# Optimization experiments

Hardware: AMD Instinct MI355X
Metric: run time of the kernel (lower is better)

Reference implementation:

```python
import jax, jax.numpy as jnp
import numpy as np

N, E, G = 50000, 1600000, 64
IN, HID, OUT = 128, 64, 64
NEG_SLOPE = 0.2


def _p(key, shape):
    return jax.random.normal(key, shape, dtype=jnp.float32) * 0.1


def setup_inputs() -> dict:
    key = jax.random.key(0)
    ks = jax.random.split(key, 24)
    inp = {
        "x": jax.random.normal(ks[0], (N, IN), dtype=jnp.float32),
        "edge_index": jax.random.randint(ks[1], (2, E), 0, N),
        "edge_attr": jax.random.uniform(ks[2], (E, 1), dtype=jnp.float32),
        "batch": jnp.sort(jax.random.randint(ks[3], (N,), 0, G)),
        # GATv2 layer 1 (in=128 -> 64, heads=1)
        "Wl1": _p(ks[4], (IN, HID)), "bl1": _p(ks[5], (HID,)),
        "Wr1": _p(ks[6], (IN, HID)), "br1": _p(ks[7], (HID,)),
        "We1": _p(ks[8], (1, HID)), "att1": _p(ks[9], (HID,)), "bias1": _p(ks[10], (HID,)),
        # GATv2 layer 2 (64 -> 64)
        "Wl2": _p(ks[11], (HID, OUT)), "bl2": _p(ks[12], (OUT,)),
        "Wr2": _p(ks[13], (HID, OUT)), "br2": _p(ks[14], (OUT,)),
        "We2": _p(ks[15], (1, OUT)), "att2": _p(ks[16], (OUT,)), "bias2": _p(ks[17], (OUT,)),
        # MLP head: fc1 (64->32), bn1 (32), fc3 (32->1)
        "W_fc1": _p(ks[18], (OUT, OUT // 2)), "b_fc1": _p(ks[19], (OUT // 2,)),
        "bn_gamma": jnp.ones((OUT // 2,), jnp.float32),
        "bn_beta": jnp.zeros((OUT // 2,), jnp.float32),
        "bn_mean": _p(ks[20], (OUT // 2,)),
        "bn_var": jax.random.uniform(ks[21], (OUT // 2,), jnp.float32, 0.5, 1.5),
        "W_fc3": _p(ks[22], (OUT // 2, 1)), "b_fc3": _p(ks[23], (1,)),
    }
    return inp


def _add_self_loops(src, dst, edge_attr, n):
    # PyG add_self_loops with fill_value='mean': loop attr = mean of incoming edge attrs per node
    s = jax.ops.segment_sum(edge_attr, dst, num_segments=n)  # (N,1)
    c = jax.ops.segment_sum(jnp.ones((edge_attr.shape[0], 1), edge_attr.dtype), dst, num_segments=n)
    loop_attr = s / jnp.maximum(c, 1.0)
    loops = jnp.arange(n)
    return (jnp.concatenate([src, loops]), jnp.concatenate([dst, loops]),
            jnp.concatenate([edge_attr, loop_attr], axis=0))


def _gatv2(h, src, dst, e_attr, Wl, bl, Wr, br, We, att, bias, n):
    xl = h @ Wl + bl                     # (N, C) source transform
    xr = h @ Wr + br                     # (N, C) target transform
    ef = e_attr @ We                     # (E', C)
    s = jax.nn.leaky_relu(xl[src] + xr[dst] + ef, NEG_SLOPE)  # (E', C)
    logits = s @ att                     # (E',)
    m = jax.ops.segment_max(logits, dst, num_segments=n)
    m = jnp.where(jnp.isfinite(m), m, 0.0)
    p = jnp.exp(logits - m[dst])
    denom = jax.ops.segment_sum(p, dst, num_segments=n)
    alpha = p / (denom[dst] + 1e-16)
    out = jax.ops.segment_sum(alpha[:, None] * xl[src], dst, num_segments=n)
    return out + bias


def reference(x, edge_index, edge_attr, batch,
              Wl1, bl1, Wr1, br1, We1, att1, bias1,
              Wl2, bl2, Wr2, br2, We2, att2, bias2,
              W_fc1, b_fc1, bn_gamma, bn_beta, bn_mean, bn_var, W_fc3, b_fc3):
    n = x.shape[0]
    src, dst, ea = _add_self_loops(edge_index[0], edge_index[1], edge_attr, n)
    h = jax.nn.elu(_gatv2(x, src, dst, ea, Wl1, bl1, Wr1, br1, We1, att1, bias1, n))
    h = jax.nn.elu(_gatv2(h, src, dst, ea, Wl2, bl2, Wr2, br2, We2, att2, bias2, n))
    # global_mean_pool
    sums = jax.ops.segment_sum(h, batch, num_segments=G)
    cnts = jax.ops.segment_sum(jnp.ones((n, 1), h.dtype), batch, num_segments=G)
    pooled = sums / jnp.maximum(cnts, 1.0)
    # head: bn1(relu(fc1(.))) with eval-mode BN, dropout off, then fc3
    z = jax.nn.relu(pooled @ W_fc1 + b_fc1)
    z = (z - bn_mean) / jnp.sqrt(bn_var + 1e-5) * bn_gamma + bn_beta
    return z @ W_fc3 + b_fc3
```

## Files before the change

kernel.cpp:

```cpp
#include <hip/hip_runtime.h>
#include <hip/hip_fp16.h>
#include <math.h>

typedef unsigned long long u64;
typedef __attribute__((ext_vector_type(2))) _Float16 half2v;
typedef __attribute__((ext_vector_type(4))) _Float16 half4v;
typedef __attribute__((ext_vector_type(8))) _Float16 half8;
typedef __attribute__((ext_vector_type(4))) float f32x4;
typedef __attribute__((ext_vector_type(2))) float f32x2;


#define BKT     256
#define CAP     12032
#define MAXSPAN 13056
#define PEPB    4096
#define NPWP    64

__global__ void k_prep_w(const float* __restrict__ Wl1, const float* __restrict__ bl1,
                         const float* __restrict__ Wr1, const float* __restrict__ br1,
                         const float* __restrict__ Wl2, const float* __restrict__ bl2,
                         const float* __restrict__ Wr2, const float* __restrict__ br2,
                         _Float16* __restrict__ Wt1, float* __restrict__ bv1,
                         _Float16* __restrict__ Wt2, float* __restrict__ bv2, int ld1) {
    int t = blockIdx.x * blockDim.x + threadIdx.x;
    int stride = gridDim.x * blockDim.x;
    int IN1 = 1 << ld1;
    for (int i = t; i < 128 * IN1; i += stride) {
        int n = i >> ld1, k = i & (IN1 - 1);
        float v = (n < 64) ? Wl1[k * 64 + n] : Wr1[k * 64 + (n - 64)];
        Wt1[n * IN1 + k] = (_Float16)v;
    }
    for (int i = t; i < 128 * 64; i += stride) {
        int n = i >> 6, k = i & 63;
        float v = (n < 64) ? Wl2[k * 64 + n] : Wr2[k * 64 + (n - 64)];
        Wt2[n * 64 + k] = (_Float16)v;
    }
    if (t < 128) {
        bv1[t] = (t < 64) ? bl1[t] : br1[t - 64];
        bv2[t] = (t < 64) ? bl2[t] : br2[t - 64];
    }
}

template<int IN>
__device__ __forceinline__ void xf_block_mfma(
        const float* __restrict__ h,
        const _Float16* __restrict__ Wt,
        const float* __restrict__ bv,
        __half* __restrict__ xl, __half* __restrict__ xr,
        int N, int node0, _Float16* rows, int t) {
    constexpr int LDK = IN + 8;
    constexpr int Q = IN / 4;
    for (int idx = t; idx < 64 * Q; idx += 256) {
        int nn = idx / Q;
        int kk = (idx % Q) * 4;
        int node = node0 + nn;
        float4 v = {0.f, 0.f, 0.f, 0.f};
        if (node < N) v = *(const float4*)(h + (size_t)node * IN + kk);
        half4v hv = {(_Float16)v.x, (_Float16)v.y, (_Float16)v.z, (_Float16)v.w};
        *(half4v*)(rows + nn * LDK + kk) = hv;
    }
    __syncthreads();
    int lane = t & 63, w = t >> 6;
    int n0w = w * 32;
    int lr = lane & 15, lq = lane >> 4;
    f32x4 acc[4][2];
#pragma unroll
    for (int i = 0; i < 4; ++i)
#pragma unroll
        for (int j = 0; j < 2; ++j) acc[i][j] = {0.f, 0.f, 0.f, 0.f};
    const _Float16* arow = rows + lr * LDK + lq * 8;
    const _Float16* brow = Wt + (size_t)(n0w + lr) * IN + lq * 8;
#pragma unroll
    for (int k0 = 0; k0 < IN; k0 += 32) {
        half8 a0 = *(const half8*)(arow + k0);
        half8 a1 = *(const half8*)(arow + 16 * LDK + k0);
        half8 a2 = *(const half8*)(arow + 32 * LDK + k0);
        half8 a3 = *(const half8*)(arow + 48 * LDK + k0);
        half8 b0 = *(const half8*)(brow + k0);
        half8 b1 = *(const half8*)(brow + 16 * IN + k0);
        acc[0][0] = __builtin_amdgcn_mfma_f32_16x16x32_f16(a0, b0, acc[0][0], 0, 0, 0);
        acc[1][0] = __builtin_amdgcn_mfma_f32_16x16x32_f16(a1, b0, acc[1][0], 0, 0, 0);
        acc[2][0] = __builtin_amdgcn_mfma_f32_16x16x32_f16(a2, b0, acc[2][0], 0, 0, 0);
        acc[3][0] = __builtin_amdgcn_mfma_f32_16x16x32_f16(a3, b0, acc[3][0], 0, 0, 0);
        acc[0][1] = __builtin_amdgcn_mfma_f32_16x16x32_f16(a0, b1, acc[0][1], 0, 0, 0);
        acc[1][1] = __builtin_amdgcn_mfma_f32_16x16x32_f16(a1, b1, acc[1][1], 0, 0, 0);
        acc[2][1] = __builtin_amdgcn_mfma_f32_16x16x32_f16(a2, b1, acc[2][1], 0, 0, 0);
        acc[3][1] = __builtin_amdgcn_mfma_f32_16x16x32_f16(a3, b1, acc[3][1], 0, 0, 0);
    }
    float bia0 = bv[n0w + lr];
    float bia1 = bv[n0w + 16 + lr];
#pragma unroll
    for (int ni = 0; ni < 2; ++ni) {
        int dim = n0w + ni * 16 + lr;
        __half* dst = (dim < 64) ? xl : xr;
        int dd = dim & 63;
        float bb = ni ? bia1 : bia0;
#pragma unroll
        for (int mi = 0; mi < 4; ++mi) {
#pragma unroll
            for (int r = 0; r < 4; ++r) {
                int node = node0 + mi * 16 + lq * 4 + r;
                if (node < N)
                    dst[((size_t)node << 6) + dd] = __float2half(acc[mi][ni][r] + bb);
            }
        }
    }
}

union XfPartSmem {
    _Float16 rows[64 * 136];
    struct { int lh[256]; int lbase[256]; int lcur[256]; } p;
};

template<int IN>
__global__ void k_xf1_part(
        const float* __restrict__ h,
        const _Float16* __restrict__ Wt, const float* __restrict__ bv,
        __half* __restrict__ xl, __half* __restrict__ xr, int N, int nbXF,
        const int* __restrict__ ei, const float* __restrict__ ea,
        int* __restrict__ qtail, u64* __restrict__ queue, int E) {
    __shared__ XfPartSmem sm;
    int t = threadIdx.x;
    if (blockIdx.x < nbXF) {
        xf_block_mfma<IN>(h, Wt, bv, xl, xr, N, blockIdx.x * 64, sm.rows, t);
    } else {
        int pb = blockIdx.x - nbXF;
        sm.p.lh[t] = 0; sm.p.lcur[t] = 0;
        __syncthreads();
        int base = pb * PEPB;
        int end = base + PEPB; if (end > E) end = E;
        for (int e = base + t; e < end; e += 256) {
            int d = ei[E + e];
            atomicAdd(&sm.p.lh[d >> 8], 1);
        }
        __syncthreads();
        if (sm.p.lh[t]) sm.p.lbase[t] = atomicAdd(&qtail[t], sm.p.lh[t]);
        __syncthreads();
        for (int e = base + t; e < end; e += 256) {
            int d = ei[E + e];
            int src = ei[e];
            float a = ea[e];
            int b = d >> 8;
            int idx = atomicAdd(&sm.p.lcur[b], 1);
            unsigned aq = (unsigned)(a * 16777216.0f);
            queue[(size_t)b * CAP + sm.p.lbase[b] + idx] =
                (((u64)aq) << 25) | (((u64)(d & 255)) << 17) | (unsigned)src;
        }
    }
}

__device__ __forceinline__ unsigned attr_q15(float a) {
    unsigned short hb = __builtin_bit_cast(unsigned short, (_Float16)a);
    return (unsigned)(hb >> 1);
}

__global__ void __launch_bounds__(1024)
k_build(const u64* __restrict__ queue, const int* __restrict__ qtail,
        u64* __restrict__ rs2, unsigned* __restrict__ csr, int N) {
    __shared__ u64 stat[BKT];
    __shared__ int fill[BKT], sc[BKT];
    __shared__ unsigned lcsr[MAXSPAN];
    int t = threadIdx.x, b = blockIdx.x;
    if (t < BKT) stat[t] = 0;
    __syncthreads();
    int cnt = qtail[b];
    size_t q0 = (size_t)b * CAP;
    for (int i = t; i < cnt; i += 1024) {
        u64 r = queue[q0 + i];
        int dl = (int)((r >> 17) & (BKT - 1));
        atomicAdd(&stat[dl], (1ULL << 32) | (unsigned)(r >> 25));
    }
    __syncthreads();
    int dg = b * BKT + t;
    u64 p = (t < BKT) ? stat[t] : 0;
    int deg = (int)(p >> 32);
    int v = (t < BKT && dg < N) ? ((deg + 1 + 3) & ~3) : 0;
    if (t < BKT) sc[t] = v;
    __syncthreads();
    for (int off = 1; off < BKT; off <<= 1) {
        int a = (t >= off && t < BKT) ? sc[t - off] : 0;
        __syncthreads();
        if (t < BKT) sc[t] += a;
        __syncthreads();
    }
    int c0 = b * MAXSPAN;
    if (t < BKT && dg < N) {
        int basel = sc[t] - v;
        rs2[dg] = (u64)(unsigned)(c0 + basel) | (((u64)(unsigned)(c0 + basel + deg + 1)) << 32);
        fill[t] = basel;
        float mean = ((float)(unsigned)p * (1.0f / 16777216.0f)) / fmaxf((float)deg, 1.0f);
        if (basel + deg < MAXSPAN) lcsr[basel + deg] = (attr_q15(mean) << 17) | (unsigned)dg;
    }
    __syncthreads();
    for (int i = t; i < cnt; i += 1024) {
        u64 r = queue[q0 + i];
        int dl = (int)((r >> 17) & (BKT - 1));
        int pos = atomicAdd(&fill[dl], 1);
        float av = (float)(unsigned)(r >> 25) * (1.0f / 16777216.0f);
        if (pos < MAXSPAN) lcsr[pos] = (attr_q15(av) << 17) | (unsigned)(r & 0x1FFFFu);
    }
    __syncthreads();
    int span = sc[BKT - 1];
    if (span > MAXSPAN) span = MAXSPAN;
    for (int j = t; j < span; j += 1024) csr[c0 + j] = lcsr[j];
}

__global__ void k_node_xf(const float* __restrict__ h,
                          const _Float16* __restrict__ Wt, const float* __restrict__ bv,
                          __half* __restrict__ xl, __half* __restrict__ xr, int N) {
    __shared__ _Float16 rows[64 * 72];
    xf_block_mfma<64>(h, Wt, bv, xl, xr, N, blockIdx.x * 64, rows, threadIdx.x);
}

template<int CTRL>
__device__ __forceinline__ float dpp_add(float c) {
    int t = __builtin_amdgcn_update_dpp(0, __builtin_bit_cast(int, c),
                                        CTRL, 0xF, 0xF, true);
    return c + __builtin_bit_cast(float, t);
}

#define EDGE_GROUP(r, xh, cc)                                                  \
    {                                                                          \
        _Float16 ah = __builtin_bit_cast(_Float16, (unsigned short)((r >> 16) & 0xFFFEu)); \
        half2v aa = {ah, ah};                                                  \
        half2v x01 = {xh.x, xh.y}, x23 = {xh.z, xh.w};                         \
        half2v v01 = aa * We01 + (x01 + xr01);                                 \
        half2v v23 = aa * We23 + (x23 + xr23);                                 \
        half2v s01 = __builtin_elementwise_max(v01, v01 * k02);                \
        half2v s23 = __builtin_elementwise_max(v23, v23 * k02);                \
        cc = __builtin_amdgcn_fdot2(s01, at01, 0.f, false);                    \
        cc = __builtin_amdgcn_fdot2(s23, at23, cc, false);                     \
    }

__global__ void k_attn(const __half* __restrict__ xl, const __half* __restrict__ xr,
                       const unsigned* __restrict__ csr, const u64* __restrict__ rs2,
                       const float* __restrict__ We, const float* __restrict__ att,
                       const float* __restrict__ bias,
                       float* __restrict__ hout, int N) {
    int lane = threadIdx.x & 63;
    int d = (int)(((size_t)blockIdx.x * blockDim.x + threadIdx.x) >> 6);
    if (d >= N) return;
    int eq = lane >> 4;
    int fl = lane & 15;
    const float LOG2E = 1.44269504088896340736f;
    float4 Wef  = *(const float4*)(We + fl * 4);
    float4 attf = *(const float4*)(att + fl * 4);
    half2v We01 = {(_Float16)Wef.x, (_Float16)Wef.y};
    half2v We23 = {(_Float16)Wef.z, (_Float16)Wef.w};
    half2v at01 = {(_Float16)(attf.x * LOG2E), (_Float16)(attf.y * LOG2E)};
    half2v at23 = {(_Float16)(attf.z * LOG2E), (_Float16)(attf.w * LOG2E)};
    unsigned flo = (unsigned)fl * 4u;
    half4v xrh = *(const half4v*)(xr + (((unsigned)d << 6) | flo));
    half2v xr01 = {xrh.x, xrh.y}, xr23 = {xrh.z, xrh.w};
    const half2v k02 = {(_Float16)0.2f, (_Float16)0.2f};
    u64 rr = rs2[d];
    int e0 = __builtin_amdgcn_readfirstlane((int)(unsigned)rr);
    int e1 = __builtin_amdgcn_readfirstlane((int)(unsigned)(rr >> 32));
    float l = 0.f;
    f32x2 Oa = {0.f, 0.f}, Ob = {0.f, 0.f};
    int e = e0;
    uint4 rv = *(const uint4*)(csr + e + (eq << 2));
    half4v xA = *(const half4v*)(xl + (((rv.x & 0x1FFFFu) << 6) | flo));
    half4v xB = *(const half4v*)(xl + (((rv.y & 0x1FFFFu) << 6) | flo));
    half4v xC = *(const half4v*)(xl + (((rv.z & 0x1FFFFu) << 6) | flo));
    half4v xD = *(const half4v*)(xl + (((rv.w & 0x1FFFFu) << 6) | flo));
    for (; e + 16 <= e1; e += 16) {
        uint4 rvn = *(const uint4*)(csr + e + 16 + (eq << 2));
        float cA, cB, cC, cD;
        EDGE_GROUP(rv.x, xA, cA);
        EDGE_GROUP(rv.y, xB, cB);
        EDGE_GROUP(rv.z, xC, cC);
        EDGE_GROUP(rv.w, xD, cD);
        half4v nA = *(const half4v*)(xl + (((rvn.x & 0x1FFFFu) << 6) | flo));
        half4v nB = *(const half4v*)(xl + (((rvn.y & 0x1FFFFu) << 6) | flo));
        half4v nC = *(const half4v*)(xl + (((rvn.z & 0x1FFFFu) << 6) | flo));
        half4v nD = *(const half4v*)(xl + (((rvn.w & 0x1FFFFu) << 6) | flo));
        cA = dpp_add<0xB1>(cA);  cB = dpp_add<0xB1>(cB);
        cC = dpp_add<0xB1>(cC);  cD = dpp_add<0xB1>(cD);
        cA = dpp_add<0x4E>(cA);  cB = dpp_add<0x4E>(cB);
        cC = dpp_add<0x4E>(cC);  cD = dpp_add<0x4E>(cD);
        cA = dpp_add<0x141>(cA); cB = dpp_add<0x141>(cB);
        cC = dpp_add<0x141>(cC); cD = dpp_add<0x141>(cD);
        cA = dpp_add<0x140>(cA); cB = dpp_add<0x140>(cB);
        cC = dpp_add<0x140>(cC); cD = dpp_add<0x140>(cD);
        float qA = __builtin_exp2f(cA), qB = __builtin_exp2f(cB);
        float qC = __builtin_exp2f(cC), qD = __builtin_exp2f(cD);
        l += (qA + qB) + (qC + qD);
        f32x2 qA2 = {qA, qA}, qB2 = {qB, qB}, qC2 = {qC, qC}, qD2 = {qD, qD};
        f32x2 xa01 = {(float)xA.x, (float)xA.y}, xa23 = {(float)xA.z, (float)xA.w};
        f32x2 xb01 = {(float)xB.x, (float)xB.y}, xb23 = {(float)xB.z, (float)xB.w};
        f32x2 xc01 = {(float)xC.x, (float)xC.y}, xc23 = {(float)xC.z, (float)xC.w};
        f32x2 xd01 = {(float)xD.x, (float)xD.y}, xd23 = {(float)xD.z, (float)xD.w};
        Oa = __builtin_elementwise_fma(qA2, xa01, Oa);
        Oa = __builtin_elementwise_fma(qB2, xb01, Oa);
        Oa = __builtin_elementwise_fma(qC2, xc01, Oa);
        Oa = __builtin_elementwise_fma(qD2, xd01, Oa);
        Ob = __builtin_elementwise_fma(qA2, xa23, Ob);
        Ob = __builtin_elementwise_fma(qB2, xb23, Ob);
        Ob = __builtin_elementwise_fma(qC2, xc23, Ob);
        Ob = __builtin_elementwise_fma(qD2, xd23, Ob);
        rv = rvn; xA = nA; xB = nB; xC = nC; xD = nD;
    }
    for (; e < e1; e += 4) {
        int ee = e + eq;
        bool valid = ee < e1;
        unsigned r = csr[valid ? ee : (e1 - 1)];
        half4v xh = *(const half4v*)(xl + (((r & 0x1FFFFu) << 6) | flo));
        float c;
        EDGE_GROUP(r, xh, c);
        c = dpp_add<0xB1>(c);
        c = dpp_add<0x4E>(c);
        c = dpp_add<0x141>(c);
        c = dpp_add<0x140>(c);
        float q = valid ? __builtin_exp2f(c) : 0.f;
        l += q;
        Oa.x = fmaf(q, (float)xh.x, Oa.x);
        Oa.y = fmaf(q, (float)xh.y, Oa.y);
        Ob.x = fmaf(q, (float)xh.z, Ob.x);
        Ob.y = fmaf(q, (float)xh.w, Ob.y);
    }
#pragma unroll
    for (int mm = 16; mm <= 32; mm <<= 1) {
        l    += __shfl_xor(l, mm, 64);
        Oa.x += __shfl_xor(Oa.x, mm, 64);
        Oa.y += __shfl_xor(Oa.y, mm, 64);
        Ob.x += __shfl_xor(Ob.x, mm, 64);
        Ob.y += __shfl_xor(Ob.y, mm, 64);
    }
    if (eq == 0) {
        float inv = 1.0f / (l + 1e-16f);
        float4 b4 = *(const float4*)(bias + fl * 4);
        float4 res;
        res.x = fmaf(Oa.x, inv, b4.x);
        res.y = fmaf(Oa.y, inv, b4.y);
        res.z = fmaf(Ob.x, inv, b4.z);
        res.w = fmaf(Ob.y, inv, b4.w);
        res.x = res.x > 0.f ? res.x : __expf(res.x) - 1.f;
        res.y = res.y > 0.f ? res.y : __expf(res.y) - 1.f;
        res.z = res.z > 0.f ? res.z : __expf(res.z) - 1.f;
        res.w = res.w > 0.f ? res.w : __expf(res.w) - 1.f;
        *(float4*)(hout + ((size_t)d << 6) + fl * 4) = res;
    }
}

__global__ void k_pool_head(const float* __restrict__ h, const int* __restrict__ batch,
                            float* __restrict__ pooled, float* __restrict__ gcnt,
                            int N, int* __restrict__ done,
                            const float* __restrict__ W1, const float* __restrict__ b1,
                            const float* __restrict__ gam, const float* __restrict__ bet,
                            const float* __restrict__ mu, const float* __restrict__ var,
                            const float* __restrict__ W3, const float* __restrict__ b3,
                            float* __restrict__ out, int G) {
    int tid = threadIdx.x;
    int lane = tid & 63;
    int wave = (int)(((size_t)blockIdx.x * blockDim.x + tid) >> 6);
    int begin = wave * NPWP;
    if (begin < N) {
        int bidx = begin + lane;
        int bval = batch[bidx < N ? bidx : (N - 1)];
        float hv[NPWP];
#pragma unroll
        for (int j = 0; j < NPWP; ++j) {
            int n = begin + j;
            hv[j] = (n < N) ? h[((size_t)n << 6) + lane] : 0.f;
        }
        int g = __shfl(bval, 0, 64);
        float acc = 0.f, cnt = 0.f;
#pragma unroll
        for (int j = 0; j < NPWP; ++j) {
            if (begin + j < N) {
                int gn = __shfl(bval, j, 64);
                if (gn != g) {
                    atomicAdd(&pooled[((size_t)g << 6) + lane], acc);
                    if (lane == 0) atomicAdd(&gcnt[g], cnt);
                    g = gn; acc = 0.f; cnt = 0.f;
                }
                acc += hv[j];
                cnt += 1.f;
            }
        }
        atomicAdd(&pooled[((size_t)g << 6) + lane], acc);
        if (lane == 0) atomicAdd(&gcnt[g], cnt);
    }
    __threadfence();
    __syncthreads();
    __shared__ int lastFlag;
    if (tid == 0) lastFlag = (atomicAdd(done, 1) == (int)gridDim.x - 1);
    __syncthreads();
    if (lastFlag && tid < G) {
        __threadfence();
        int g = tid;
        float inv = 1.0f / fmaxf(gcnt[g], 1.0f);
        float pr[64];
        for (int k = 0; k < 64; ++k) pr[k] = pooled[((size_t)g << 6) + k] * inv;
        float o = b3[0];
        for (int j = 0; j < 32; ++j) {
            float z = b1[j];
            for (int k = 0; k < 64; ++k) z += pr[k] * W1[k * 32 + j];
            z = fmaxf(z, 0.f);
            z = (z - mu[j]) / sqrtf(var[j] + 1e-5f) * gam[j] + bet[j];
            o += z * W3[j];
        }
        out[g] = o;
    }
}

extern "C" void kernel_launch(void* const* d_in, const int* in_sizes, int n_in,
                              void* d_out, int out_size, void* d_ws, size_t ws_size,
                              hipStream_t stream) {
    const float* x    = (const float*)d_in[0];
    const int*   ei   = (const int*)d_in[1];
    const float* ea   = (const float*)d_in[2];
    const int*   batch= (const int*)d_in[3];
    const float* Wl1  = (const float*)d_in[4];
    const float* bl1  = (const float*)d_in[5];
    const float* Wr1  = (const float*)d_in[6];
    const float* br1  = (const float*)d_in[7];
    const float* We1  = (const float*)d_in[8];
    const float* att1 = (const float*)d_in[9];
    const float* bi1  = (const float*)d_in[10];
    const float* Wl2  = (const float*)d_in[11];
    const float* bl2  = (const float*)d_in[12];
    const float* Wr2  = (const float*)d_in[13];
    const float* br2  = (const float*)d_in[14];
    const float* We2  = (const float*)d_in[15];
    const float* att2 = (const float*)d_in[16];
    const float* bi2  = (const float*)d_in[17];
    const float* Wf1  = (const float*)d_in[18];
    const float* bf1  = (const float*)d_in[19];
    const float* gam  = (const float*)d_in[20];
    const float* bet  = (const float*)d_in[21];
    const float* mu   = (const float*)d_in[22];
    const float* var  = (const float*)d_in[23];
    const float* Wf3  = (const float*)d_in[24];
    const float* bf3  = (const float*)d_in[25];

    const int N    = in_sizes[3];
    const int E    = in_sizes[2];
    const int INd  = in_sizes[0] / N;
    const int ld1  = (INd == 128) ? 7 : 6;
    const int G    = out_size;
    const int NB   = (N + BKT - 1) / BKT;

    char* w = (char*)d_ws;
    auto carve = [&](size_t bytes) { char* p = w; w += (bytes + 255) & ~(size_t)255; return p; };
    __half*   xl       = (__half*)  carve((size_t)N * 64 * 2);
    __half*   xr       = (__half*)  carve((size_t)N * 64 * 2);
    float*    hbuf     = (float*)   carve((size_t)N * 64 * 4);
    unsigned* csr      = (unsigned*)carve(((size_t)NB * MAXSPAN + 256) * 4);
    u64*      queue    = (u64*)     carve((size_t)NB * CAP * 8);
    u64*      rs2      = (u64*)     carve((size_t)N * 8);
    int*      qtail    = (int*)     carve((size_t)(NB + 1) * 4);
    float*    pooled   = (float*)   carve((size_t)G * 64 * 4);
    float*    gcnt     = (float*)   carve((size_t)G * 4);
    int*      done     = (int*)     carve(256);
    _Float16* Wt1      = (_Float16*)carve((size_t)128 * 128 * 2);
    float*    bv1      = (float*)   carve(128 * 4);
    _Float16* Wt2      = (_Float16*)carve((size_t)128 * 64 * 2);
    float*    bv2      = (float*)   carve(128 * 4);

    const int TB = 256;
    const int nbXF = (N + 63) / 64;
    const int attnBlocks = (N + 3) / 4;
    const int nbPart = (E + PEPB - 1) / PEPB;

    hipMemsetAsync(qtail, 0, (size_t)(NB + 1) * 4, stream);
    size_t poolRegion = (((size_t)G * 64 * 4 + 255) & ~(size_t)255)
                      + (((size_t)G * 4 + 255) & ~(size_t)255) + 256;
    hipMemsetAsync(pooled, 0, poolRegion, stream);

    k_prep_w<<<32, TB, 0, stream>>>(Wl1, bl1, Wr1, br1, Wl2, bl2, Wr2, br2,
                                    Wt1, bv1, Wt2, bv2, ld1);

    if (INd == 128)
        k_xf1_part<128><<<nbXF + nbPart, TB, 0, stream>>>(x, Wt1, bv1, xl, xr, N, nbXF,
                                                          ei, ea, qtail, queue, E);
    else
        k_xf1_part<64><<<nbXF + nbPart, TB, 0, stream>>>(x, Wt1, bv1, xl, xr, N, nbXF,
                                                         ei, ea, qtail, queue, E);
    k_build<<<NB, 1024, 0, stream>>>(queue, qtail, rs2, csr, N);

    k_attn<<<attnBlocks, TB, 0, stream>>>(xl, xr, csr, rs2, We1, att1, bi1, hbuf, N);

    k_node_xf<<<nbXF, TB, 0, stream>>>(hbuf, Wt2, bv2, xl, xr, N);
    k_attn<<<attnBlocks, TB, 0, stream>>>(xl, xr, csr, rs2, We2, att2, bi2, hbuf, N);

    const int poolWaves = (N + NPWP - 1) / NPWP;
    k_pool_head<<<(poolWaves * 64 + TB - 1) / TB, TB, 0, stream>>>(
        hbuf, batch, pooled, gcnt, N, done,
        Wf1, bf1, gam, bet, mu, var, Wf3, bf3, (float*)d_out, G);
}
```

Before: 303.9 us.

## Store layer activations in fp16, preload build records, merge zeroing memsets

The intermediate activation buffer between the GAT layers and pooling is now stored as fp16 instead of fp32. This halves the write traffic from the attention kernels and the read traffic in the second transform and in pooling. k_build now loads its queue records into registers once (up to 12 per thread) and reuses them for both the histogram and scatter passes, avoiding a second global read. The two zeroing memsets are merged into one contiguous memset. The trade-offs are extra rounding of the ELU outputs before pooling and a fixed per-thread capacity of 12288 records that silently drops records if a bucket exceeds it (CAP is 12032, so it fits).

```diff
diff --git a/kernel.cpp b/kernel.cpp
--- a/kernel.cpp
+++ b/kernel.cpp
@@ -41,9 +41,9 @@
     }
 }
 
-template<int IN>
+template<int IN, bool F32IN>
 __device__ __forceinline__ void xf_block_mfma(
-        const float* __restrict__ h,
+        const void* __restrict__ hsrc,
         const _Float16* __restrict__ Wt,
         const float* __restrict__ bv,
         __half* __restrict__ xl, __half* __restrict__ xr,
@@ -54,9 +54,15 @@
         int nn = idx / Q;
         int kk = (idx % Q) * 4;
         int node = node0 + nn;
-        float4 v = {0.f, 0.f, 0.f, 0.f};
-        if (node < N) v = *(const float4*)(h + (size_t)node * IN + kk);
-        half4v hv = {(_Float16)v.x, (_Float16)v.y, (_Float16)v.z, (_Float16)v.w};
+        half4v hv = {(_Float16)0.f, (_Float16)0.f, (_Float16)0.f, (_Float16)0.f};
+        if (node < N) {
+            if constexpr (F32IN) {
+                float4 v = *(const float4*)((const float*)hsrc + (size_t)node * IN + kk);
+                hv = half4v{(_Float16)v.x, (_Float16)v.y, (_Float16)v.z, (_Float16)v.w};
+            } else {
+                hv = *(const half4v*)((const _Float16*)hsrc + (size_t)node * IN + kk);
+            }
+        }
         *(half4v*)(rows + nn * LDK + kk) = hv;
     }
     __syncthreads();
@@ -122,7 +128,7 @@
     __shared__ XfPartSmem sm;
     int t = threadIdx.x;
     if (blockIdx.x < nbXF) {
-        xf_block_mfma<IN>(h, Wt, bv, xl, xr, N, blockIdx.x * 64, sm.rows, t);
+        xf_block_mfma<IN, true>(h, Wt, bv, xl, xr, N, blockIdx.x * 64, sm.rows, t);
     } else {
         int pb = blockIdx.x - nbXF;
         sm.p.lh[t] = 0; sm.p.lcur[t] = 0;
@@ -165,10 +171,20 @@
     __syncthreads();
     int cnt = qtail[b];
     size_t q0 = (size_t)b * CAP;
-    for (int i = t; i < cnt; i += 1024) {
-        u64 r = queue[q0 + i];
-        int dl = (int)((r >> 17) & (BKT - 1));
-        atomicAdd(&stat[dl], (1ULL << 32) | (unsigned)(r >> 25));
+    u64 rec[12];
+#pragma unroll
+    for (int k = 0; k < 12; ++k) {
+        int i = t + k * 1024;
+        rec[k] = (i < cnt) ? queue[q0 + i] : 0;
+    }
+#pragma unroll
+    for (int k = 0; k < 12; ++k) {
+        int i = t + k * 1024;
+        if (i < cnt) {
+            u64 r = rec[k];
+            atomicAdd(&stat[(int)((r >> 17) & (BKT - 1))],
+                      (1ULL << 32) | (unsigned)(r >> 25));
+        }
     }
     __syncthreads();
     int dg = b * BKT + t;
@@ -192,12 +208,16 @@
         if (basel + deg < MAXSPAN) lcsr[basel + deg] = (attr_q15(mean) << 17) | (unsigned)dg;
     }
     __syncthreads();
-    for (int i = t; i < cnt; i += 1024) {
-        u64 r = queue[q0 + i];
-        int dl = (int)((r >> 17) & (BKT - 1));
-        int pos = atomicAdd(&fill[dl], 1);
-        float av = (float)(unsigned)(r >> 25) * (1.0f / 16777216.0f);
-        if (pos < MAXSPAN) lcsr[pos] = (attr_q15(av) << 17) | (unsigned)(r & 0x1FFFFu);
+#pragma unroll
+    for (int k = 0; k < 12; ++k) {
+        int i = t + k * 1024;
+        if (i < cnt) {
+            u64 r = rec[k];
+            int dl = (int)((r >> 17) & (BKT - 1));
+            int pos = atomicAdd(&fill[dl], 1);
+            float av = (float)(unsigned)(r >> 25) * (1.0f / 16777216.0f);
+            if (pos < MAXSPAN) lcsr[pos] = (attr_q15(av) << 17) | (unsigned)(r & 0x1FFFFu);
+        }
     }
     __syncthreads();
     int span = sc[BKT - 1];
@@ -205,11 +225,11 @@
     for (int j = t; j < span; j += 1024) csr[c0 + j] = lcsr[j];
 }
 
-__global__ void k_node_xf(const float* __restrict__ h,
+__global__ void k_node_xf(const __half* __restrict__ h,
                           const _Float16* __restrict__ Wt, const float* __restrict__ bv,
                           __half* __restrict__ xl, __half* __restrict__ xr, int N) {
     __shared__ _Float16 rows[64 * 72];
-    xf_block_mfma<64>(h, Wt, bv, xl, xr, N, blockIdx.x * 64, rows, threadIdx.x);
+    xf_block_mfma<64, false>(h, Wt, bv, xl, xr, N, blockIdx.x * 64, rows, threadIdx.x);
 }
 
 template<int CTRL>
@@ -236,7 +256,7 @@
                        const unsigned* __restrict__ csr, const u64* __restrict__ rs2,
                        const float* __restrict__ We, const float* __restrict__ att,
                        const float* __restrict__ bias,
-                       float* __restrict__ hout, int N) {
+                       __half* __restrict__ hout, int N) {
     int lane = threadIdx.x & 63;
     int d = (int)(((size_t)blockIdx.x * blockDim.x + threadIdx.x) >> 6);
     if (d >= N) return;
@@ -339,11 +359,12 @@
         res.y = res.y > 0.f ? res.y : __expf(res.y) - 1.f;
         res.z = res.z > 0.f ? res.z : __expf(res.z) - 1.f;
         res.w = res.w > 0.f ? res.w : __expf(res.w) - 1.f;
-        *(float4*)(hout + ((size_t)d << 6) + fl * 4) = res;
-    }
-}
-
-__global__ void k_pool_head(const float* __restrict__ h, const int* __restrict__ batch,
+        half4v rh = {(_Float16)res.x, (_Float16)res.y, (_Float16)res.z, (_Float16)res.w};
+        *(half4v*)(hout + (((size_t)d << 6) | flo)) = rh;
+    }
+}
+
+__global__ void k_pool_head(const __half* __restrict__ h, const int* __restrict__ batch,
                             float* __restrict__ pooled, float* __restrict__ gcnt,
                             int N, int* __restrict__ done,
                             const float* __restrict__ W1, const float* __restrict__ b1,
@@ -362,7 +383,7 @@
 #pragma unroll
         for (int j = 0; j < NPWP; ++j) {
             int n = begin + j;
-            hv[j] = (n < N) ? h[((size_t)n << 6) + lane] : 0.f;
+            hv[j] = (n < N) ? __half2float(h[((size_t)n << 6) + lane]) : 0.f;
         }
         int g = __shfl(bval, 0, 64);
         float acc = 0.f, cnt = 0.f;
@@ -446,14 +467,16 @@
     auto carve = [&](size_t bytes) { char* p = w; w += (bytes + 255) & ~(size_t)255; return p; };
     __half*   xl       = (__half*)  carve((size_t)N * 64 * 2);
     __half*   xr       = (__half*)  carve((size_t)N * 64 * 2);
-    float*    hbuf     = (float*)   carve((size_t)N * 64 * 4);
+    __half*   hbuf     = (__half*)  carve((size_t)N * 64 * 2);
     unsigned* csr      = (unsigned*)carve(((size_t)NB * MAXSPAN + 256) * 4);
     u64*      queue    = (u64*)     carve((size_t)NB * CAP * 8);
     u64*      rs2      = (u64*)     carve((size_t)N * 8);
+    char*     z0       = w;
     int*      qtail    = (int*)     carve((size_t)(NB + 1) * 4);
     float*    pooled   = (float*)   carve((size_t)G * 64 * 4);
     float*    gcnt     = (float*)   carve((size_t)G * 4);
     int*      done     = (int*)     carve(256);
+    size_t    zbytes   = (size_t)(w - z0);
     _Float16* Wt1      = (_Float16*)carve((size_t)128 * 128 * 2);
     float*    bv1      = (float*)   carve(128 * 4);
     _Float16* Wt2      = (_Float16*)carve((size_t)128 * 64 * 2);
@@ -464,10 +487,7 @@
     const int attnBlocks = (N + 3) / 4;
     const int nbPart = (E + PEPB - 1) / PEPB;
 
-    hipMemsetAsync(qtail, 0, (size_t)(NB + 1) * 4, stream);
-    size_t poolRegion = (((size_t)G * 64 * 4 + 255) & ~(size_t)255)
-                      + (((size_t)G * 4 + 255) & ~(size_t)255) + 256;
-    hipMemsetAsync(pooled, 0, poolRegion, stream);
+    hipMemsetAsync(z0, 0, zbytes, stream);
 
     k_prep_w<<<32, TB, 0, stream>>>(Wl1, bl1, Wr1, br1, Wl2, bl2, Wr2, br2,
                                     Wt1, bv1, Wt2, bv2, ld1);
```

Result: slower. 319.2 us (+5.1%).
